# Performance work log

Measured on AMD Instinct MI355X. Metric: run time of the kernel, lower is better.

## Reference

```python
import jax, jax.numpy as jnp
import numpy as np
from functools import partial

B, N, NCLS = 16, 25200, 80
M_TGT = 50
MAX_DET = 300
CONF_THRES = 0.8
NMS_THRES = 0.4


def cxcywh_to_xyxy(boxes):
    # cxcywh -> xywh -> xyxy (as in tensor_to_dict: cxcywh_to_xywh then xywh_to_xyxy)
    cx, cy, w, h = boxes[..., 0], boxes[..., 1], boxes[..., 2], boxes[..., 3]
    x1 = cx - 0.5 * w
    y1 = cy - 0.5 * h
    return jnp.stack([x1, y1, x1 + w, y1 + h], axis=-1)


def pairwise_iou(b):
    # b: [K,4] xyxy
    x1 = jnp.maximum(b[:, None, 0], b[None, :, 0])
    y1 = jnp.maximum(b[:, None, 1], b[None, :, 1])
    x2 = jnp.minimum(b[:, None, 2], b[None, :, 2])
    y2 = jnp.minimum(b[:, None, 3], b[None, :, 3])
    inter = jnp.clip(x2 - x1, 0.0) * jnp.clip(y2 - y1, 0.0)
    area = jnp.clip(b[:, 2] - b[:, 0], 0.0) * jnp.clip(b[:, 3] - b[:, 1], 0.0)
    return inter / (area[:, None] + area[None, :] - inter + 1e-9)


def nms_one(boxes_xyxy, labels, valid):
    # boxes sorted by score descending; class-aware greedy NMS, fixed K iterations
    K = boxes_xyxy.shape[0]
    iou = pairwise_iou(boxes_xyxy)
    same = labels[:, None] == labels[None, :]
    supp = (iou > NMS_THRES) & same
    idx = jnp.arange(K)

    def body(i, keep):
        kill = supp[i] & (idx > i) & keep[i]
        return keep & ~kill

    return jax.lax.fori_loop(0, K, body, valid)


def post_process(preds):
    # preds: [B, N, 5+C] (cx,cy,w,h,obj,cls...)
    obj = preds[..., 4]
    cls_prob = preds[..., 5:]
    cls_conf = jnp.max(cls_prob, axis=-1)
    cls_id = jnp.argmax(cls_prob, axis=-1)
    score = obj * cls_conf                      # [B,N]
    score = jnp.where(score > CONF_THRES, score, 0.0)
    top_s, top_i = jax.lax.top_k(score, MAX_DET)            # [B,K]
    boxes = jnp.take_along_axis(preds[..., :4], top_i[..., None], axis=1)  # cxcywh [B,K,4]
    labels = jnp.take_along_axis(cls_id, top_i, axis=1)     # [B,K]
    valid = top_s > 0.0
    boxes_xyxy = cxcywh_to_xyxy(boxes)
    keep = jax.vmap(nms_one)(boxes_xyxy, labels, valid)     # [B,K]
    scores = jnp.where(keep, top_s, 0.0)
    boxes_xyxy = jnp.where(keep[..., None], boxes_xyxy, 0.0)
    labels = jnp.where(keep, labels, -1)
    return boxes_xyxy, scores, labels, keep


def process_targets(tt, lengths):
    # tt: [B, M, 6] = cxcywh, score, label ; lengths: [B]
    valid = jnp.arange(tt.shape[1])[None, :] < lengths[:, None]  # [B,M]
    boxes = cxcywh_to_xyxy(tt[..., :4])
    scores = tt[..., 4]
    labels = tt[..., 5].astype(jnp.int32)
    boxes = jnp.where(valid[..., None], boxes, 0.0)
    scores = jnp.where(valid, scores, 0.0)
    labels = jnp.where(valid, labels, -1)
    return boxes, scores, labels, valid


def setup_inputs() -> dict:
    key = jax.random.key(0)
    k1, k2, k3, k4 = jax.random.split(key, 4)
    preds = jax.random.uniform(k1, (B, N, 5 + NCLS), dtype=jnp.float32)
    tgt_boxes = jax.random.uniform(k2, (B, M_TGT, 4), dtype=jnp.float32) * 640.0
    tgt_scores = jnp.ones((B, M_TGT, 1), dtype=jnp.float32)
    tgt_labels = jax.random.randint(k3, (B, M_TGT, 1), 0, NCLS).astype(jnp.float32)
    target_target = jnp.concatenate([tgt_boxes, tgt_scores, tgt_labels], axis=-1)
    target_lengths = jax.random.randint(k4, (B,), 1, M_TGT + 1).astype(jnp.int32)
    return {"preds": preds, "target_target": target_target, "target_lengths": target_lengths}


def reference(preds, target_target, target_lengths):
    pb, ps, pl, pv = post_process(preds)
    tb, ts, tl, tv = process_targets(target_target, target_lengths)
    # @torch.no_grad in original forward
    out = (pb, ps, pl, pv, tb, ts, tl, tv)
    return jax.tree_util.tree_map(jax.lax.stop_gradient, out)
```

## Files before the change

### kernel.cpp

```cpp
#include <hip/hip_runtime.h>
#include <cstdint>

#define BB 16
#define NN 25200
#define NCLS 80
#define NF (5 + NCLS)
#define MAXDET 300
#define MTGT 50
#define CONF 0.8f
#define NMSTH 0.4f
#define WORDS 10
#define NBINS 2048
#define CAPALL 8192
#define SBUF 2048
#define APB 64
#define CHUNK_V4 (APB * NF / 4)
#define SCORE_BLOCKS ((BB * NN) / APB)
#define NTGT_BLOCKS ((BB * MTGT + 127) / 128)
#define HSTRIDE 33

#define WS_SCORE 0

#define O_PB 0
#define O_PS (BB * MAXDET * 4)
#define O_PL (O_PS + BB * MAXDET)
#define O_PV (O_PL + BB * MAXDET)
#define O_TB (O_PV + BB * MAXDET)
#define O_TS (O_TB + BB * MTGT * 4)
#define O_TL (O_TS + BB * MTGT)
#define O_TV (O_TL + BB * MTGT)

__global__ __launch_bounds__(128) void k_score(const float* __restrict__ preds,
                                               float* __restrict__ scores,
                                               const float* __restrict__ tt,
                                               const int* __restrict__ len,
                                               float* __restrict__ out) {
    __shared__ float st[APB * NF];
    int tid = threadIdx.x;
    int bid = blockIdx.x;

    if (bid >= SCORE_BLOCKS) {
        int t = (bid - SCORE_BLOCKS) * 128 + tid;
        if (t < BB * MTGT) {
            int b = t / MTGT, m = t - b * MTGT;
            const float* row = tt + (size_t)t * 6;
            bool valid = m < len[b];
            float cx = row[0], cy = row[1], w = row[2], h = row[3];
            float x1 = cx - 0.5f * w, y1 = cy - 0.5f * h;
            float* tb = out + O_TB + (size_t)t * 4;
            tb[0] = valid ? x1 : 0.f;
            tb[1] = valid ? y1 : 0.f;
            tb[2] = valid ? (x1 + w) : 0.f;
            tb[3] = valid ? (y1 + h) : 0.f;
            out[O_TS + t] = valid ? row[4] : 0.f;
            out[O_TL + t] = valid ? (float)(int)row[5] : -1.f;
            out[O_TV + t] = valid ? 1.f : 0.f;
        }
        return;
    }

    int w = tid >> 6;
    const float4* src = (const float4*)(preds + (size_t)bid * (APB * NF));
    #pragma unroll
    for (int i = 0; i < 11; ++i) {
        int idx = i * 128 + tid;
        if (idx < CHUNK_V4) {
            __builtin_amdgcn_global_load_lds(
                (const __attribute__((address_space(1))) void*)(src + idx),
                (__attribute__((address_space(3))) void*)(st + (i * 128 + w * 64) * 4),
                16, 0, 0);
        }
    }
    __syncthreads();

    int a = tid >> 1, h = tid & 1;
    const float* cls = st + a * NF + 5 + h * 40;
    float m0 = cls[0], m1 = cls[1], m2 = cls[2], m3 = cls[3];
    #pragma unroll
    for (int f = 4; f < 40; f += 4) {
        m0 = fmaxf(m0, cls[f]);     m1 = fmaxf(m1, cls[f + 1]);
        m2 = fmaxf(m2, cls[f + 2]); m3 = fmaxf(m3, cls[f + 3]);
    }
    float m = fmaxf(fmaxf(m0, m1), fmaxf(m2, m3));
    m = fmaxf(m, __shfl_xor(m, 1));
    if (h == 0) scores[bid * APB + a] = st[a * NF + 4] * m;
}

__global__ __launch_bounds__(1024) void k_post(const float* __restrict__ scores,
                                               const float* __restrict__ preds,
                                               float* __restrict__ out) {
    __shared__ unsigned long long skall[CAPALL];
    __shared__ unsigned long long sk[SBUF];
    __shared__ unsigned long long skTop[MAXDET];
    __shared__ int hist[64 * HSTRIDE];
    __shared__ float4   sbox[MAXDET];
    __shared__ int      slabel[MAXDET];
    __shared__ float    sscore[MAXDET];
    __shared__ unsigned supp[MAXDET * WORDS];
    __shared__ int wsum[16];
    __shared__ int lcnt, lcnt2, scut;
    int b = blockIdx.x;
    int tid = threadIdx.x;
    int lane = tid & 63;
    int wv = tid >> 6;

    if (tid == 0) { lcnt = 0; lcnt2 = 0; }
    for (int i = tid; i < 64 * HSTRIDE; i += 1024) hist[i] = 0;
    if (tid < MAXDET) skTop[tid] = 0ull;
    __syncthreads();

    const float4* src4 = (const float4*)(scores + (size_t)b * NN);
    float4 r[7];
    #pragma unroll
    for (int i = 0; i < 7; ++i) {
        int idx = i * 1024 + tid;
        r[i] = make_float4(0.f, 0.f, 0.f, 0.f);
        if (idx < NN / 4) r[i] = src4[idx];
    }
    int cnt = 0;
    #pragma unroll
    for (int i = 0; i < 7; ++i) {
        #pragma unroll
        for (int c = 0; c < 4; ++c) {
            float s = (c == 0) ? r[i].x : (c == 1) ? r[i].y : (c == 2) ? r[i].z : r[i].w;
            if (s > CONF) {
                ++cnt;
                unsigned u = __float_as_uint(s);
                int bin = (int)((u - 0x3F400000u) >> 12);
                bin = bin < 0 ? 0 : (bin > NBINS - 1 ? NBINS - 1 : bin);
                atomicAdd(&hist[(bin >> 5) * HSTRIDE + (bin & 31)], 1);
            }
        }
    }
    int inc = cnt;
    #pragma unroll
    for (int d = 1; d < 64; d <<= 1) {
        int o = __shfl_up(inc, d);
        if (lane >= d) inc += o;
    }
    if (lane == 63) wsum[wv] = inc;
    __syncthreads();
    int wbase = 0;
    #pragma unroll
    for (int q = 0; q < 16; ++q) wbase += (q < wv) ? wsum[q] : 0;
    int base = wbase + inc - cnt;
    if (tid == 1023) lcnt = wbase + inc;
    {
        int p = base;
        #pragma unroll
        for (int i = 0; i < 7; ++i) {
            int idx = i * 1024 + tid;
            #pragma unroll
            for (int c = 0; c < 4; ++c) {
                float s = (c == 0) ? r[i].x : (c == 1) ? r[i].y : (c == 2) ? r[i].z : r[i].w;
                if (s > CONF) {
                    if (p < CAPALL) {
                        unsigned u = __float_as_uint(s);
                        skall[p] = ((unsigned long long)u << 32) |
                                   (unsigned long long)(0xFFFFFFFFu - (unsigned)(4 * idx + c));
                    }
                    ++p;
                }
            }
        }
    }
    __syncthreads();

    if (tid < 64) {
        int sb = 0;
        #pragma unroll
        for (int k = 0; k < 32; ++k) sb += hist[lane * HSTRIDE + k];
        int cum = sb;
        #pragma unroll
        for (int d = 1; d < 64; d <<= 1) {
            int o = __shfl_down(cum, d);
            if (lane + d < 64) cum += o;
        }
        unsigned long long m = __ballot(cum >= MAXDET);
        int cutbin = 0;
        if (m) {
            int cutS = 63 - __clzll(m);
            int tail = (cutS < 63) ? __shfl(cum, cutS + 1) : 0;
            int hh = (lane < 32) ? hist[cutS * HSTRIDE + lane] : 0;
            int c2 = hh;
            #pragma unroll
            for (int d = 1; d < 32; d <<= 1) {
                int o = __shfl_down(c2, d);
                if (lane + d < 32) c2 += o;
            }
            c2 += tail;
            unsigned long long m2 = __ballot(lane < 32 && c2 >= MAXDET);
            int cutL = 63 - __clzll(m2);
            cutbin = cutS * 32 + cutL;
        }
        if (lane == 0) scut = cutbin;
    }
    __syncthreads();
    int cutbin = scut;

    int M = lcnt; if (M > CAPALL) M = CAPALL;
    for (int i = tid; i < ((M + 1023) & ~1023); i += 1024) {
        bool pass = false;
        unsigned long long key = 0ull;
        if (i < M) {
            key = skall[i];
            unsigned u = (unsigned)(key >> 32);
            int bin = (int)((u - 0x3F400000u) >> 12);
            bin = bin < 0 ? 0 : (bin > NBINS - 1 ? NBINS - 1 : bin);
            pass = bin >= cutbin;
        }
        unsigned long long mask = __ballot(pass);
        int wcnt = __popcll(mask);
        int bs = 0;
        if (lane == 0 && wcnt) bs = atomicAdd(&lcnt2, wcnt);
        bs = __shfl(bs, 0);
        if (pass) {
            int pos = bs + __popcll(mask & ((1ull << lane) - 1ull));
            if (pos < SBUF) sk[pos] = key;
        }
    }
    __syncthreads();

    int M2 = lcnt2; if (M2 > SBUF) M2 = SBUF;
    for (int c = tid; c < M2; c += 1024) {
        unsigned long long key = sk[c];
        int rank = 0;
        for (int j = 0; j < M2; ++j) rank += (sk[j] > key) ? 1 : 0;
        if (rank < MAXDET) skTop[rank] = key;
    }
    __syncthreads();

    {
        int k = tid >> 1, h = tid & 1;
        if (k < MAXDET) {
            unsigned long long key = skTop[k];
            unsigned sbits = (unsigned)(key >> 32);
            if (sbits) {
                int idx = (int)(0xFFFFFFFFu - (unsigned)(key & 0xFFFFFFFFu));
                const float* row = preds + ((size_t)b * NN + (size_t)idx) * NF;
                const float* cls = row + 5 + h * 40;
                float v = cls[0]; int ci = h * 40;
                #pragma unroll
                for (int f = 1; f < 40; ++f) {
                    float x = cls[f];
                    if (x > v) { v = x; ci = h * 40 + f; }
                }
                float ov = __shfl_xor(v, 1);
                int   oi = __shfl_xor(ci, 1);
                if (ov > v || (ov == v && oi < ci)) { v = ov; ci = oi; }
                if (h == 0) {
                    float cx = row[0], cy = row[1], w = row[2], hh = row[3];
                    float x1 = cx - 0.5f * w, y1 = cy - 0.5f * hh;
                    float4 bx = { x1, y1, x1 + w, y1 + hh };
                    sbox[k] = bx;
                    slabel[k] = ci;
                    sscore[k] = __uint_as_float(sbits);
                }
            } else if (h == 0) {
                float4 zz = { 0.f, 0.f, 0.f, 0.f };
                sbox[k] = zz; slabel[k] = -1; sscore[k] = 0.f;
            }
        }
    }
    __syncthreads();

    for (int T = tid; T < MAXDET * WORDS; T += 1024) {
        int i  = T / WORDS;
        int jw = T - i * WORDS;
        unsigned word = 0;
        int jbase = jw * 32;
        if (jbase + 31 > i) {
            float4 bi = sbox[i];
            int   li = slabel[i];
            float si = sscore[i];
            float ai = __fmul_rn(fmaxf(__fsub_rn(bi.z, bi.x), 0.f),
                                 fmaxf(__fsub_rn(bi.w, bi.y), 0.f));
            for (int uu = 0; uu < 32; ++uu) {
                int t = (uu + jw) & 31;
                int j = jbase + t;
                if (j > i && j < MAXDET) {
                    if (slabel[j] == li && si > 0.f && sscore[j] > 0.f) {
                        float4 bj = sbox[j];
                        float xx1 = fmaxf(bi.x, bj.x);
                        float yy1 = fmaxf(bi.y, bj.y);
                        float xx2 = fminf(bi.z, bj.z);
                        float yy2 = fminf(bi.w, bj.w);
                        float iw = fmaxf(__fsub_rn(xx2, xx1), 0.f);
                        float ih = fmaxf(__fsub_rn(yy2, yy1), 0.f);
                        float inter = __fmul_rn(iw, ih);
                        float aj = __fmul_rn(fmaxf(__fsub_rn(bj.z, bj.x), 0.f),
                                             fmaxf(__fsub_rn(bj.w, bj.y), 0.f));
                        float den = __fadd_rn(__fsub_rn(__fadd_rn(ai, aj), inter), 1e-9f);
                        float iou = inter / den;
                        if (iou > NMSTH) word |= 1u << t;
                    }
                }
            }
        }
        supp[T] = word;
    }
    __syncthreads();

    if (tid < 64) {
        unsigned keep = 0, nzm = 0;
        #pragma unroll
        for (int s = 0; s < 5; ++s) {
            int k = s * 64 + lane;
            bool kb = (k < MAXDET) && (sscore[k] > 0.f);
            unsigned long long m = __ballot(kb);
            if (lane == 2 * s)     keep = (unsigned)m;
            if (lane == 2 * s + 1) keep = (unsigned)(m >> 32);
            unsigned nz = 0;
            if (k < MAXDET) {
                #pragma unroll
                for (int w = 0; w < WORDS; ++w) nz |= supp[k * WORDS + w];
            }
            unsigned long long mn = __ballot(nz != 0u);
            if (lane == 2 * s)     nzm = (unsigned)mn;
            if (lane == 2 * s + 1) nzm = (unsigned)(mn >> 32);
        }

        for (int i = 0; i < MAXDET; ++i) {
            int idx = i >> 5;
            unsigned kw = __shfl(keep, idx);
            unsigned nw = __shfl(nzm, idx);
            if (((kw & nw) >> (i & 31)) & 1u) {
                if (lane < WORDS) keep &= ~supp[i * WORDS + lane];
            }
        }

        #pragma unroll
        for (int s = 0; s < 5; ++s) {
            int k = s * 64 + lane;
            if (k < MAXDET) {
                unsigned kw = __shfl(keep, k >> 5);
                bool kp = (kw >> (k & 31)) & 1u;
                int g = b * MAXDET + k;
                float4 bx = sbox[k];
                float4 zz = { 0.f, 0.f, 0.f, 0.f };
                ((float4*)(out + O_PB))[g] = kp ? bx : zz;
                out[O_PS + g] = kp ? sscore[k] : 0.f;
                out[O_PL + g] = kp ? (float)slabel[k] : -1.f;
                out[O_PV + g] = kp ? 1.f : 0.f;
            }
        }
    }
}

extern "C" void kernel_launch(void* const* d_in, const int* in_sizes, int n_in,
                              void* d_out, int out_size, void* d_ws, size_t ws_size,
                              hipStream_t stream) {
    const float* preds = (const float*)d_in[0];
    const float* tt    = (const float*)d_in[1];
    const int*   len   = (const int*)d_in[2];
    float* out = (float*)d_out;

    float* scores = (float*)((char*)d_ws + WS_SCORE);

    k_score<<<SCORE_BLOCKS + NTGT_BLOCKS, 128, 0, stream>>>(preds, scores, tt, len, out);
    k_post <<<BB, 1024, 0, stream>>>(scores, preds, out);
}
```

Measured before the change: 79.24 us.

## Compact above-threshold candidates per block in score kernel instead of writing dense scores

The score kernel now filters anchors against the confidence threshold with a wave ballot. Each block writes up to 48 packed score/index keys and a per-block count into the workspace, and blocks are laid out so each batch owns a fixed range of 394 blocks. The post kernel reads only the counts and compacted keys and builds the histogram from them, instead of scanning all 25200 dense scores per batch in a single block. This cuts the serial global read and threshold work in the 16-block post kernel. In exchange it adds a per-thread uncoalesced copy loop over each block's key slot, and a fixed 48-key cap per 64 anchors that could silently drop candidates on unusual inputs.

Result: no change. 78.91 us (-0.4%).

```diff
diff --git a/kernel.cpp b/kernel.cpp
--- a/kernel.cpp
+++ b/kernel.cpp
@@ -14,12 +14,14 @@
 #define CAPALL 8192
 #define SBUF 2048
 #define APB 64
-#define CHUNK_V4 (APB * NF / 4)
-#define SCORE_BLOCKS ((BB * NN) / APB)
+#define CPB 394
+#define SLOTK 48
+#define SCORE_BLOCKS (BB * CPB)
 #define NTGT_BLOCKS ((BB * MTGT + 127) / 128)
 #define HSTRIDE 33
 
-#define WS_SCORE 0
+#define WS_CNTS 0
+#define WS_KEYS 32768
 
 #define O_PB 0
 #define O_PS (BB * MAXDET * 4)
@@ -31,11 +33,13 @@
 #define O_TV (O_TL + BB * MTGT)
 
 __global__ __launch_bounds__(128) void k_score(const float* __restrict__ preds,
-                                               float* __restrict__ scores,
+                                               int* __restrict__ cnts,
+                                               unsigned long long* __restrict__ keys,
                                                const float* __restrict__ tt,
                                                const int* __restrict__ len,
                                                float* __restrict__ out) {
     __shared__ float st[APB * NF];
+    __shared__ int wbase0;
     int tid = threadIdx.x;
     int bid = blockIdx.x;
 
@@ -59,12 +63,18 @@
         return;
     }
 
+    int b  = bid / CPB;
+    int cb = bid - b * CPB;
+    int count = (cb == CPB - 1) ? (NN - (CPB - 1) * APB) : APB;
+    int nv4 = count * NF / 4;
+
     int w = tid >> 6;
-    const float4* src = (const float4*)(preds + (size_t)bid * (APB * NF));
+    int lane = tid & 63;
+    const float4* src = (const float4*)(preds + ((size_t)b * NN + (size_t)cb * APB) * NF);
     #pragma unroll
     for (int i = 0; i < 11; ++i) {
         int idx = i * 128 + tid;
-        if (idx < CHUNK_V4) {
+        if (idx < nv4) {
             __builtin_amdgcn_global_load_lds(
                 (const __attribute__((address_space(1))) void*)(src + idx),
                 (__attribute__((address_space(3))) void*)(st + (i * 128 + w * 64) * 4),
@@ -83,10 +93,31 @@
     }
     float m = fmaxf(fmaxf(m0, m1), fmaxf(m2, m3));
     m = fmaxf(m, __shfl_xor(m, 1));
-    if (h == 0) scores[bid * APB + a] = st[a * NF + 4] * m;
+    float s = st[a * NF + 4] * m;
+
+    bool pass = (h == 0) && (a < count) && (s > CONF);
+    unsigned long long mask = __ballot(pass);
+    int wcnt = __popcll(mask);
+    if (w == 0 && lane == 0) wbase0 = wcnt;
+    __syncthreads();
+    int base = (w == 0) ? 0 : wbase0;
+    if (pass) {
+        int pos = base + __popcll(mask & ((1ull << lane) - 1ull));
+        if (pos < SLOTK) {
+            unsigned u = __float_as_uint(s);
+            keys[(size_t)bid * SLOTK + pos] =
+                ((unsigned long long)u << 32) |
+                (unsigned long long)(0xFFFFFFFFu - (unsigned)(cb * APB + a));
+        }
+    }
+    if (w == 1 && lane == 0) {
+        int tot = base + wcnt;
+        cnts[bid] = tot < SLOTK ? tot : SLOTK;
+    }
 }
 
-__global__ __launch_bounds__(1024) void k_post(const float* __restrict__ scores,
+__global__ __launch_bounds__(1024) void k_post(const int* __restrict__ cnts,
+                                               const unsigned long long* __restrict__ keys,
                                                const float* __restrict__ preds,
                                                float* __restrict__ out) {
     __shared__ unsigned long long skall[CAPALL];
@@ -109,30 +140,8 @@
     if (tid < MAXDET) skTop[tid] = 0ull;
     __syncthreads();
 
-    const float4* src4 = (const float4*)(scores + (size_t)b * NN);
-    float4 r[7];
-    #pragma unroll
-    for (int i = 0; i < 7; ++i) {
-        int idx = i * 1024 + tid;
-        r[i] = make_float4(0.f, 0.f, 0.f, 0.f);
-        if (idx < NN / 4) r[i] = src4[idx];
-    }
-    int cnt = 0;
-    #pragma unroll
-    for (int i = 0; i < 7; ++i) {
-        #pragma unroll
-        for (int c = 0; c < 4; ++c) {
-            float s = (c == 0) ? r[i].x : (c == 1) ? r[i].y : (c == 2) ? r[i].z : r[i].w;
-            if (s > CONF) {
-                ++cnt;
-                unsigned u = __float_as_uint(s);
-                int bin = (int)((u - 0x3F400000u) >> 12);
-                bin = bin < 0 ? 0 : (bin > NBINS - 1 ? NBINS - 1 : bin);
-                atomicAdd(&hist[(bin >> 5) * HSTRIDE + (bin & 31)], 1);
-            }
-        }
-    }
-    int inc = cnt;
+    int c = (tid < CPB) ? cnts[b * CPB + tid] : 0;
+    int inc = c;
     #pragma unroll
     for (int d = 1; d < 64; d <<= 1) {
         int o = __shfl_up(inc, d);
@@ -143,26 +152,22 @@
     int wbase = 0;
     #pragma unroll
     for (int q = 0; q < 16; ++q) wbase += (q < wv) ? wsum[q] : 0;
-    int base = wbase + inc - cnt;
+    int base = wbase + inc - c;
     if (tid == 1023) lcnt = wbase + inc;
-    {
-        int p = base;
-        #pragma unroll
-        for (int i = 0; i < 7; ++i) {
-            int idx = i * 1024 + tid;
-            #pragma unroll
-            for (int c = 0; c < 4; ++c) {
-                float s = (c == 0) ? r[i].x : (c == 1) ? r[i].y : (c == 2) ? r[i].z : r[i].w;
-                if (s > CONF) {
-                    if (p < CAPALL) {
-                        unsigned u = __float_as_uint(s);
-                        skall[p] = ((unsigned long long)u << 32) |
-                                   (unsigned long long)(0xFFFFFFFFu - (unsigned)(4 * idx + c));
-                    }
-                    ++p;
-                }
-            }
-        }
+    if (tid < CPB) {
+        const unsigned long long* slot = keys + (size_t)(b * CPB + tid) * SLOTK;
+        for (int k = 0; k < c; ++k) {
+            int p = base + k;
+            if (p < CAPALL) skall[p] = slot[k];
+        }
+    }
+    __syncthreads();
+    int M = lcnt; if (M > CAPALL) M = CAPALL;
+    for (int i = tid; i < M; i += 1024) {
+        unsigned u = (unsigned)(skall[i] >> 32);
+        int bin = (int)((u - 0x3F400000u) >> 12);
+        bin = bin < 0 ? 0 : (bin > NBINS - 1 ? NBINS - 1 : bin);
+        atomicAdd(&hist[(bin >> 5) * HSTRIDE + (bin & 31)], 1);
     }
     __syncthreads();
 
@@ -198,7 +203,6 @@
     __syncthreads();
     int cutbin = scut;
 
-    int M = lcnt; if (M > CAPALL) M = CAPALL;
     for (int i = tid; i < ((M + 1023) & ~1023); i += 1024) {
         bool pass = false;
         unsigned long long key = 0ull;
@@ -222,8 +226,8 @@
     __syncthreads();
 
     int M2 = lcnt2; if (M2 > SBUF) M2 = SBUF;
-    for (int c = tid; c < M2; c += 1024) {
-        unsigned long long key = sk[c];
+    for (int c2 = tid; c2 < M2; c2 += 1024) {
+        unsigned long long key = sk[c2];
         int rank = 0;
         for (int j = 0; j < M2; ++j) rank += (sk[j] > key) ? 1 : 0;
         if (rank < MAXDET) skTop[rank] = key;
@@ -355,8 +359,10 @@
     const int*   len   = (const int*)d_in[2];
     float* out = (float*)d_out;
 
-    float* scores = (float*)((char*)d_ws + WS_SCORE);
-
-    k_score<<<SCORE_BLOCKS + NTGT_BLOCKS, 128, 0, stream>>>(preds, scores, tt, len, out);
-    k_post <<<BB, 1024, 0, stream>>>(scores, preds, out);
+    char* ws = (char*)d_ws;
+    int* cnts = (int*)(ws + WS_CNTS);
+    unsigned long long* keys = (unsigned long long*)(ws + WS_KEYS);
+
+    k_score<<<SCORE_BLOCKS + NTGT_BLOCKS, 128, 0, stream>>>(preds, cnts, keys, tt, len, out);
+    k_post <<<BB, 1024, 0, stream>>>(cnts, keys, preds, out);
 }
```
